# Performance work log

Hardware: AMD Instinct MI355X
Metric: run time of the kernel (lower is better)

Reference implementation:

```python
import jax, jax.numpy as jnp
import numpy as np

NTYPES = 2
B, N, MNEI = 4, 512, 100
M = MNEI * NTYPES          # neighbor slots = maxNeighborNum * ntypes
EMB_LAST = 100             # embedding net sizes [25, 50, 100]
FIT_H = 240
M2 = 16
RMIN, RMAX = 0.5, 6.0


def setup_inputs():
    key = jax.random.key(0)
    ks = jax.random.split(key, 24)
    r = jax.random.uniform(ks[0], (B, N, M), minval=0.6, maxval=7.0)
    v = jax.random.normal(ks[1], (B, N, M, 3))
    v = v / jnp.linalg.norm(v, axis=-1, keepdims=True)
    keep = jax.random.uniform(ks[2], (B, N, M)) < 0.7
    ImageDR = jnp.concatenate([r[..., None], r[..., None] * v], axis=-1)
    ImageDR = jnp.where(keep[..., None], ImageDR, 0.0).astype(jnp.float32)
    Imagetype_map = jax.random.randint(ks[3], (N,), 0, NTYPES)
    list_neigh = jax.random.randint(ks[4], (B, N, M), 0, N + 1)
    type_map = jnp.arange(NTYPES)
    davg = (0.01 * jax.random.normal(ks[5], (NTYPES, M, 4))).astype(jnp.float32)
    dstd = (1.0 + 0.1 * jax.random.uniform(ks[6], (NTYPES, M, 4))).astype(jnp.float32)

    def w(k, shape, fan):
        return (jax.random.normal(k, shape) / np.sqrt(fan)).astype(jnp.float32)

    def b(k, shape):
        return (0.1 * jax.random.normal(k, shape)).astype(jnp.float32)

    emb_W0 = w(ks[7], (NTYPES, NTYPES, 1, 25), 1)
    emb_b0 = b(ks[8], (NTYPES, NTYPES, 25))
    emb_W1 = w(ks[9], (NTYPES, NTYPES, 25, 50), 25)
    emb_b1 = b(ks[10], (NTYPES, NTYPES, 50))
    emb_W2 = w(ks[11], (NTYPES, NTYPES, 50, 100), 50)
    emb_b2 = b(ks[12], (NTYPES, NTYPES, 100))
    fin = M2 * EMB_LAST
    fit_W0 = w(ks[13], (NTYPES, fin, FIT_H), fin)
    fit_b0 = b(ks[14], (NTYPES, FIT_H))
    fit_W1 = w(ks[15], (NTYPES, FIT_H, FIT_H), FIT_H)
    fit_b1 = b(ks[16], (NTYPES, FIT_H))
    fit_W2 = w(ks[17], (NTYPES, FIT_H, FIT_H), FIT_H)
    fit_b2 = b(ks[18], (NTYPES, FIT_H))
    fit_W3 = w(ks[19], (NTYPES, FIT_H, 1), FIT_H)
    fit_b3 = b(ks[20], (NTYPES, 1))
    energy_shift = jnp.array([-3.37, -5.21], dtype=jnp.float32)
    return dict(list_neigh=list_neigh, Imagetype_map=Imagetype_map, type_map=type_map,
                ImageDR=ImageDR, nghost=0, davg=davg, dstd=dstd,
                emb_W0=emb_W0, emb_b0=emb_b0, emb_W1=emb_W1, emb_b1=emb_b1,
                emb_W2=emb_W2, emb_b2=emb_b2,
                fit_W0=fit_W0, fit_b0=fit_b0, fit_W1=fit_W1, fit_b1=fit_b1,
                fit_W2=fit_W2, fit_b2=fit_b2, fit_W3=fit_W3, fit_b3=fit_b3,
                energy_shift=energy_shift)


def _emb(s, W0, b0, W1, b1, W2, b2):
    # DeepPot-SE embedding net with doubling resnet connections
    h = jnp.tanh(s @ W0 + b0)                                   # [..., 25]
    h = jnp.tanh(h @ W1 + b1) + jnp.concatenate([h, h], -1)     # [..., 50]
    return jnp.tanh(h @ W2 + b2) + jnp.concatenate([h, h], -1)  # [..., 100]


def _fit(d, W0, b0, W1, b1, W2, b2, W3, b3):
    h = jnp.tanh(d @ W0 + b0)
    h = h + jnp.tanh(h @ W1 + b1)
    h = h + jnp.tanh(h @ W2 + b2)
    return h @ W3 + b3


def _forward(ImageDR, davg, dstd,
             emb_W0, emb_b0, emb_W1, emb_b1, emb_W2, emb_b2,
             fit_W0, fit_b0, fit_W1, fit_b1, fit_W2, fit_b2, fit_W3, fit_b3,
             energy_shift, Imagetype_map):
    Bsz, Nat, Mtot, _ = ImageDR.shape
    m = Mtot // NTYPES
    R = ImageDR[..., 0]
    Rsafe = jnp.where(R > 1e-5, R, 1.0)
    # smooth switching function s(r): 1/r below Rmin, polynomial taper to Rmax
    u = (R - RMIN) / (RMAX - RMIN)
    mid = (u ** 3 * (-6.0 * u * u + 15.0 * u - 10.0) + 1.0) / Rsafe
    S = jnp.where((R > 0) & (R < RMIN), 1.0 / Rsafe,
                  jnp.where((R > RMIN) & (R < RMAX), mid, 0.0))
    msk = (jnp.abs(R) > 1e-5)[..., None]
    Ri = jnp.concatenate([S[..., None],
                          jnp.where(msk, (S / Rsafe)[..., None] * ImageDR[..., 1:4], 0.0)],
                         axis=-1)                                    # [B,N,M,4] = (s, s*x/r, s*y/r, s*z/r)
    # per-center-type normalization (irregular gather of stats)
    Rn = (Ri - davg[Imagetype_map][None]) / dstd[Imagetype_map][None]
    tmask = [(Imagetype_map == i).astype(Rn.dtype)[None, :, None, None] for i in range(NTYPES)]
    xyz = jnp.zeros((Bsz, Nat, 4, EMB_LAST), Rn.dtype)
    for j in range(NTYPES):                                          # neighbor-type slice
        sl = Rn[:, :, j * m:(j + 1) * m, :]                          # [B,N,m,4]
        s = sl[..., 0:1]
        G = jnp.zeros(sl.shape[:3] + (EMB_LAST,), sl.dtype)
        for i in range(NTYPES):                                      # center type -> pair net (i, j)
            G = G + tmask[i] * _emb(s, emb_W0[i, j], emb_b0[i, j],
                                    emb_W1[i, j], emb_b1[i, j], emb_W2[i, j], emb_b2[i, j])
        xyz = xyz + jnp.einsum('bnmk,bnmc->bnkc', sl, G)
    xyz = xyz / (m * NTYPES)
    # descriptor D = (Ri^T G)^T (Ri^T G)[:, :M2], flattened -> [B,N,EMB_LAST*M2]
    D = jnp.einsum('bnkc,bnkd->bncd', xyz, xyz[..., :M2]).reshape(Bsz, Nat, -1)
    Ei = jnp.zeros((Bsz, Nat), D.dtype)
    for i in range(NTYPES):
        e = _fit(D, fit_W0[i], fit_b0[i], fit_W1[i], fit_b1[i],
                 fit_W2[i], fit_b2[i], fit_W3[i], fit_b3[i])[..., 0] + energy_shift[i]
        Ei = Ei + tmask[i][:, :, 0, 0] * e
    Etot = jnp.sum(Ei, axis=1)
    return Etot, Ei


def reference(list_neigh, Imagetype_map, type_map, ImageDR, nghost, davg, dstd,
              emb_W0, emb_b0, emb_W1, emb_b1, emb_W2, emb_b2,
              fit_W0, fit_b0, fit_W1, fit_b1, fit_W2, fit_b2, fit_W3, fit_b3,
              energy_shift):
    return _forward(ImageDR, davg, dstd,
                    emb_W0, emb_b0, emb_W1, emb_b1, emb_W2, emb_b2,
                    fit_W0, fit_b0, fit_W1, fit_b1, fit_W2, fit_b2, fit_W3, fit_b3,
                    energy_shift, Imagetype_map)
```

## Files before the change

kernel.cpp:

```cpp
#include <hip/hip_runtime.h>
#include <math.h>

#define NT 2
#define BSZ 4
#define NAT 512
#define NATOMS 2048
#define NNEI 200
#define EMB 100
#define FITH 240
#define DDIM 1600
#define TBK 1024

#define BIAS_F  16
#define W3C_F   (BIAS_F + 3 * 512)
#define PERM_I  2064
#define CNT_I   (PERM_I + 2048)
#define USH_BYTE 16512
#define TBL_U   0
#define W0T_U   409600
#define W1T_U   (W0T_U + 819200)
#define W2T_U   (W1T_U + 262144)
#define D_U     (W2T_U + 262144)
#define H0_U    (D_U + 3276800)
#define H1_U    (H0_U + 1048576)
#define USH_END (H1_U + 1048576)
#define WS_NEED ((size_t)USH_BYTE + (size_t)USH_END * 2)

#define N_W0 819200
#define N_W1 262144
#define N_W2 262144
#define N_B  1536
#define N_W3 512
#define N_EI 2048
#define N_WT (N_W0 + N_W1 + N_W2 + N_B + N_W3 + N_EI)
#define WT_BLK ((N_WT + 255) / 256)
#define TB_BLK 512

#define HPAD 264

typedef short s8v __attribute__((ext_vector_type(8)));
typedef float f4v __attribute__((ext_vector_type(4)));

__device__ __forceinline__ float ftanh(float x) {
    float ax = fabsf(x);
    float e = __expf(2.0f * ax);
    float t = 1.0f - __fdividef(2.0f, e + 1.0f);
    return (x < 0.0f) ? -t : t;
}
__device__ __forceinline__ unsigned short f2bf(float f) {
    unsigned u = __float_as_uint(f);
    u += 0x7FFFu + ((u >> 16) & 1u);
    return (unsigned short)(u >> 16);
}
__device__ __forceinline__ float bf2f(unsigned short s) {
    return __uint_as_float(((unsigned)s) << 16);
}
__device__ __forceinline__ float calc_S(float R) {
    float Rsafe = (R > 1e-5f) ? R : 1.0f;
    float u = (R - 0.5f) * (1.0f / 5.5f);
    float uu = u * u;
    float mid = (u * uu * (-6.0f * uu + 15.0f * u - 10.0f) + 1.0f) / Rsafe;
    float S = 0.0f;
    if (R > 0.0f && R < 0.5f)      S = 1.0f / Rsafe;
    else if (R > 0.5f && R < 6.0f) S = mid;
    return S;
}

__global__ void __launch_bounds__(256) prep_kernel(
    const float* __restrict__ fW0, const float* __restrict__ fW1,
    const float* __restrict__ fW2,
    const float* __restrict__ fb0, const float* __restrict__ fb1,
    const float* __restrict__ fb2,
    const float* __restrict__ fW3, const float* __restrict__ fb3,
    const float* __restrict__ eshift,
    const float* __restrict__ davg, const float* __restrict__ dstd,
    const float* __restrict__ eW0, const float* __restrict__ eb0,
    const float* __restrict__ eW1, const float* __restrict__ eb1,
    const float* __restrict__ eW2, const float* __restrict__ eb2,
    const int* __restrict__ itype,
    float* __restrict__ ws, float* __restrict__ out)
{
    __shared__ float los[100], his[100];
    __shared__ float rng[2];
    __shared__ float h0s[8][25];
    __shared__ float h1s[8][50];
    __shared__ int pcnt, poff0, poff1;
    const int tid = threadIdx.x;
    int bxg = blockIdx.x;
    unsigned short* u0 = (unsigned short*)((char*)ws + USH_BYTE);

    if (bxg < WT_BLK) {
        int id = bxg * 256 + tid;
        if (id < N_W0) {
            int n = id / 1600, k = id - n * 1600;
            float v = 0.0f;
            if (n < 240)                  v = fW0[(size_t)k * 240 + n];
            else if (n >= 256 && n < 496) v = fW0[(size_t)(1600 + k) * 240 + (n - 256)];
            u0[W0T_U + id] = f2bf(v);
            return;
        }
        id -= N_W0;
        if (id < N_W1) {
            int n = id / 512, k = id - n * 512;
            float v = 0.0f;
            if (n < 240 && k < 240)       v = fW1[(size_t)k * 240 + n];
            else if (n >= 256 && n < 496 && k >= 256 && k < 496)
                                          v = fW1[(size_t)(240 + (k - 256)) * 240 + (n - 256)];
            u0[W1T_U + id] = f2bf(v);
            return;
        }
        id -= N_W1;
        if (id < N_W2) {
            int n = id / 512, k = id - n * 512;
            float v = 0.0f;
            if (n < 240 && k < 240)       v = fW2[(size_t)k * 240 + n];
            else if (n >= 256 && n < 496 && k >= 256 && k < 496)
                                          v = fW2[(size_t)(240 + (k - 256)) * 240 + (n - 256)];
            u0[W2T_U + id] = f2bf(v);
            return;
        }
        id -= N_W2;
        if (id < N_B) {
            int l = id / 512, n = id - l * 512;
            const float* fb = (l == 0) ? fb0 : (l == 1) ? fb1 : fb2;
            float v = 0.0f;
            if (n < 240)                  v = fb[n];
            else if (n >= 256 && n < 496) v = fb[240 + (n - 256)];
            ws[BIAS_F + l * 512 + n] = v;
            return;
        }
        id -= N_B;
        if (id < N_W3) {
            int n = id;
            float v = 0.0f;
            if (n < 240)                  v = fW3[n];
            else if (n >= 256 && n < 496) v = fW3[240 + (n - 256)];
            ws[W3C_F + n] = v;
            return;
        }
        id -= N_W3;
        if (id < N_EI) {
            int t = itype[id & (NAT - 1)];
            out[4 + id] = fb3[t] + eshift[t];
        }
        return;
    }
    bxg -= WT_BLK;
    if (bxg < TB_BLK) {
        const int nid = bxg >> 7;
        const int kb  = (bxg & 127) * 8;
        const int t = nid >> 1, j = nid & 1;
        if (tid < 100) {
            int m = j * 100 + tid;
            float av = davg[(t * NNEI + m) * 4];
            float sd = dstd[(t * NNEI + m) * 4];
            float inv = __fdividef(1.0f, sd);
            float a = (0.0f - av) * inv;
            float b = (2.0f - av) * inv;
            los[tid] = fminf(a, b);
            his[tid] = fmaxf(a, b);
        }
        __syncthreads();
        if (tid == 0) {
            float lo = los[0], hi = his[0];
            for (int i = 1; i < 100; ++i) { lo = fminf(lo, los[i]); hi = fmaxf(hi, his[i]); }
            rng[0] = lo; rng[1] = hi - lo;
            if (kb == 0) {
                ws[nid * 2] = lo;
                ws[nid * 2 + 1] = (float)(TBK - 1) / (hi - lo);
            }
        }
        __syncthreads();
        const float smin = rng[0], span = rng[1];
        const float* W0 = eW0 + nid * 25;
        const float* B0 = eb0 + nid * 25;
        if (tid < 200) {
            int q = tid / 25, a = tid % 25;
            float s = smin + span * ((float)(kb + q) * (1.0f / (TBK - 1)));
            h0s[q][a] = ftanh(fmaf(s, W0[a], B0[a]));
        }
        __syncthreads();
        const float* W1 = eW1 + nid * 1250;
        const float* B1 = eb1 + nid * 50;
        for (int idx = tid; idx < 400; idx += 256) {
            int q = idx / 50, cc = idx % 50;
            float acc = B1[cc];
#pragma unroll
            for (int a = 0; a < 25; ++a) acc = fmaf(h0s[q][a], W1[a * 50 + cc], acc);
            h1s[q][cc] = ftanh(acc) + h0s[q][(cc < 25) ? cc : cc - 25];
        }
        __syncthreads();
        const float* W2 = eW2 + nid * 5000;
        const float* B2 = eb2 + nid * 100;
        unsigned short* tblu = u0 + TBL_U;
        for (int idx = tid; idx < 800; idx += 256) {
            int q = idx / 100, c = idx % 100;
            float acc = B2[c];
#pragma unroll
            for (int a = 0; a < 50; ++a) acc = fmaf(h1s[q][a], W2[a * 100 + c], acc);
            float g = ftanh(acc) + h1s[q][(c < 50) ? c : c - 50];
            tblu[(size_t)(nid * TBK + kb + q) * 100 + c] = f2bf(g);
        }
        return;
    }
    if (tid == 0) { pcnt = 0; poff0 = 0; poff1 = 0; }
    __syncthreads();
    int* wsi = (int*)ws;
    int local0 = 0;
    for (int i = tid; i < NATOMS; i += 256) local0 += (itype[i & (NAT - 1)] == 0);
    atomicAdd(&pcnt, local0);
    __syncthreads();
    const int c0 = pcnt;
    for (int i = tid; i < NATOMS; i += 256) {
        int t = itype[i & (NAT - 1)];
        int pos = (t == 0) ? atomicAdd(&poff0, 1) : (c0 + atomicAdd(&poff1, 1));
        wsi[PERM_I + pos] = i;
    }
    if (tid == 0) { wsi[CNT_I] = c0; wsi[CNT_I + 1] = NATOMS - c0; }
}

__global__ void __launch_bounds__(128) embed_kernel(
    const int* __restrict__ itype, const float* __restrict__ imagedr,
    const float* __restrict__ davg, const float* __restrict__ dstd,
    float* __restrict__ ws)
{
    __shared__ __align__(16) float4 srn[NNEI];
    __shared__ float sx[NNEI];
    __shared__ float part[2][400];
    const int atom = blockIdx.x;
    const int n = atom & (NAT - 1);
    const int tid = threadIdx.x;
    const int t = itype[n];
    unsigned short* u0 = (unsigned short*)((char*)ws + USH_BYTE);

    const float sm0 = ws[(t * 2 + 0) * 2], sc0 = ws[(t * 2 + 0) * 2 + 1];
    const float sm1 = ws[(t * 2 + 1) * 2], sc1 = ws[(t * 2 + 1) * 2 + 1];

    for (int m = tid; m < NNEI; m += 128) {
        float4 dr = ((const float4*)imagedr)[(size_t)atom * NNEI + m];
        float R = dr.x;
        float S = calc_S(R);
        float Rsafe = (R > 1e-5f) ? R : 1.0f;
        float sr = (fabsf(R) > 1e-5f) ? (S / Rsafe) : 0.0f;
        float4 av = ((const float4*)davg)[t * NNEI + m];
        float4 sd = ((const float4*)dstd)[t * NNEI + m];
        float4 rv;
        rv.x = (S         - av.x) / sd.x;
        rv.y = (sr * dr.y - av.y) / sd.y;
        rv.z = (sr * dr.z - av.z) / sd.z;
        rv.w = (sr * dr.w - av.w) / sd.w;
        srn[m] = rv;
        float smin = (m >= 100) ? sm1 : sm0;
        float scal = (m >= 100) ? sc1 : sc0;
        sx[m] = fminf(fmaxf((rv.x - smin) * scal, 0.0f), (float)(TBK - 2) + 0.9999f);
    }
    __syncthreads();

    const int w = tid >> 6, lane = tid & 63;
    const unsigned short* T = u0 + TBL_U + (size_t)(t * 2 + w) * TBK * EMB;
    const bool hi = (lane < 36);
    float xA0 = 0, xA1 = 0, xA2 = 0, xA3 = 0;
    float xB0 = 0, xB1 = 0, xB2 = 0, xB3 = 0;
#pragma unroll 4
    for (int mi = 0; mi < 100; ++mi) {
        int m = w * 100 + mi;
        float4 rv = srn[m];
        float x = sx[m];
        int i = (int)x;
        float f = x - (float)i;
        const unsigned short* Tr = T + (size_t)i * EMB;
        float g0 = bf2f(Tr[lane]);
        float g1 = bf2f(Tr[EMB + lane]);
        float g = fmaf(f, g1 - g0, g0);
        xA0 = fmaf(rv.x, g, xA0); xA1 = fmaf(rv.y, g, xA1);
        xA2 = fmaf(rv.z, g, xA2); xA3 = fmaf(rv.w, g, xA3);
        if (hi) {
            float h0v = bf2f(Tr[64 + lane]);
            float h1v = bf2f(Tr[EMB + 64 + lane]);
            float g2 = fmaf(f, h1v - h0v, h0v);
            xB0 = fmaf(rv.x, g2, xB0); xB1 = fmaf(rv.y, g2, xB1);
            xB2 = fmaf(rv.z, g2, xB2); xB3 = fmaf(rv.w, g2, xB3);
        }
    }
    part[w][0 * 100 + lane] = xA0; part[w][1 * 100 + lane] = xA1;
    part[w][2 * 100 + lane] = xA2; part[w][3 * 100 + lane] = xA3;
    if (hi) {
        part[w][0 * 100 + 64 + lane] = xB0; part[w][1 * 100 + 64 + lane] = xB1;
        part[w][2 * 100 + 64 + lane] = xB2; part[w][3 * 100 + 64 + lane] = xB3;
    }
    __syncthreads();
    const float inv = 1.0f / 200.0f;
    for (int idx = tid; idx < 400; idx += 128)
        part[0][idx] = (part[0][idx] + part[1][idx]) * inv;
    __syncthreads();
    unsigned short* Drow = u0 + D_U + (size_t)atom * DDIM;
    const float* xt = part[0];
    for (int idx = tid; idx < DDIM; idx += 128) {
        int c = idx >> 4, d = idx & 15;
        float s = xt[c] * xt[d] + xt[100 + c] * xt[100 + d]
                + xt[200 + c] * xt[200 + d] + xt[300 + c] * xt[300 + d];
        Drow[idx] = f2bf(s);
    }
}

__device__ __forceinline__ void fit_gemm256(
    const unsigned short* Hsrc, const unsigned short* Bp,
    int h, int mr, int q, f4v acc[4])
{
#pragma unroll
    for (int kt = 0; kt < 4; ++kt) {
        s8v av = *(const s8v*)((const char*)Hsrc
                 + (size_t)mr * (HPAD * 2) + h * 256 + q * 16 + kt * 64);
#pragma unroll
        for (int j = 0; j < 4; ++j) {
            s8v b = *(const s8v*)(Bp + j * 16 * 512 + kt * 32);
            acc[j] = __builtin_amdgcn_mfma_f32_16x16x32_bf16(av, b, acc[j], 0, 0, 0);
        }
    }
}

__global__ void __launch_bounds__(512) fit_kernel(
    const unsigned short* __restrict__ A,
    const unsigned short* __restrict__ W0T,
    const unsigned short* __restrict__ W1T,
    const unsigned short* __restrict__ W2T,
    const float* __restrict__ biases,
    const float* __restrict__ w3c,
    const int* __restrict__ wsi,
    float* __restrict__ out)
{
    __shared__ float lred[4][64][17];
    __shared__ unsigned short Hs0[16 * HPAD];
    __shared__ unsigned short Hs1[16 * HPAD];
    __shared__ float red2[16][4];

    const int z = blockIdx.y;
    const int cnt = wsi[CNT_I + z];
    const int my = blockIdx.x;
    if (my * 16 >= cnt) return;
    const int base = z ? wsi[CNT_I] : 0;
    const int tid = threadIdx.x;
    const int w = tid >> 6, lane = tid & 63;
    const int mr = lane & 15, q = lane >> 4;
    const int wc = w & 3, h = w >> 2;
    const int n0 = z * 256 + wc * 64;
    const int m0 = my * 16;
    const int arow = wsi[PERM_I + base + min(m0 + mr, cnt - 1)];

    {
        const unsigned short* Ap = A   + (size_t)arow * DDIM + h * 800 + q * 8;
        const unsigned short* Bp = W0T + (size_t)(n0 + mr) * DDIM + h * 800 + q * 8;
        f4v a0 = {0,0,0,0}, a1 = {0,0,0,0}, a2 = {0,0,0,0}, a3 = {0,0,0,0};
#pragma unroll 5
        for (int kt = 0; kt < 25; ++kt) {
            s8v av = *(const s8v*)(Ap + kt * 32);
            s8v b0 = *(const s8v*)(Bp + kt * 32);
            s8v b1 = *(const s8v*)(Bp + 16 * DDIM + kt * 32);
            s8v b2 = *(const s8v*)(Bp + 32 * DDIM + kt * 32);
            s8v b3 = *(const s8v*)(Bp + 48 * DDIM + kt * 32);
            a0 = __builtin_amdgcn_mfma_f32_16x16x32_bf16(av, b0, a0, 0, 0, 0);
            a1 = __builtin_amdgcn_mfma_f32_16x16x32_bf16(av, b1, a1, 0, 0, 0);
            a2 = __builtin_amdgcn_mfma_f32_16x16x32_bf16(av, b2, a2, 0, 0, 0);
            a3 = __builtin_amdgcn_mfma_f32_16x16x32_bf16(av, b3, a3, 0, 0, 0);
        }
        if (h == 1) {
#pragma unroll
            for (int r = 0; r < 4; ++r) {
                lred[wc][lane][r]      = a0[r];
                lred[wc][lane][4 + r]  = a1[r];
                lred[wc][lane][8 + r]  = a2[r];
                lred[wc][lane][12 + r] = a3[r];
            }
        }
        __syncthreads();
        if (h == 0) {
#pragma unroll
            for (int j = 0; j < 4; ++j) {
                const float bv = biases[n0 + j * 16 + mr];
                f4v* ap = (j == 0) ? &a0 : (j == 1) ? &a1 : (j == 2) ? &a2 : &a3;
#pragma unroll
                for (int r = 0; r < 4; ++r) {
                    float s = (*ap)[r] + lred[wc][lane][j * 4 + r] + bv;
                    int row = q * 4 + r, col = wc * 64 + j * 16 + mr;
                    Hs0[row * HPAD + col] = f2bf(ftanh(s));
                }
            }
        }
        __syncthreads();
    }

    {
        const unsigned short* Bp = W1T + (size_t)(n0 + mr) * 512 + z * 256 + h * 128 + q * 8;
        f4v acc[4] = {{0,0,0,0},{0,0,0,0},{0,0,0,0},{0,0,0,0}};
        fit_gemm256(Hs0, Bp, h, mr, q, acc);
        if (h == 1) {
#pragma unroll
            for (int j = 0; j < 4; ++j)
#pragma unroll
                for (int r = 0; r < 4; ++r) lred[wc][lane][j * 4 + r] = acc[j][r];
        }
        __syncthreads();
        if (h == 0) {
#pragma unroll
            for (int j = 0; j < 4; ++j) {
                const float bv = biases[512 + n0 + j * 16 + mr];
#pragma unroll
                for (int r = 0; r < 4; ++r) {
                    float s = acc[j][r] + lred[wc][lane][j * 4 + r] + bv;
                    int row = q * 4 + r, col = wc * 64 + j * 16 + mr;
                    float hv = bf2f(Hs0[row * HPAD + col]) + ftanh(s);
                    Hs1[row * HPAD + col] = f2bf(hv);
                }
            }
        }
        __syncthreads();
    }

    {
        const unsigned short* Bp = W2T + (size_t)(n0 + mr) * 512 + z * 256 + h * 128 + q * 8;
        f4v acc[4] = {{0,0,0,0},{0,0,0,0},{0,0,0,0},{0,0,0,0}};
        fit_gemm256(Hs1, Bp, h, mr, q, acc);
        if (h == 1) {
#pragma unroll
            for (int j = 0; j < 4; ++j)
#pragma unroll
                for (int r = 0; r < 4; ++r) lred[wc][lane][j * 4 + r] = acc[j][r];
        }
        __syncthreads();
        if (h == 0) {
            float pr[4] = {0, 0, 0, 0};
#pragma unroll
            for (int j = 0; j < 4; ++j) {
                const int col = n0 + j * 16 + mr;
                const float bv = biases[1024 + col];
                const float wv = w3c[col];
#pragma unroll
                for (int r = 0; r < 4; ++r) {
                    float s = acc[j][r] + lred[wc][lane][j * 4 + r] + bv;
                    int row = q * 4 + r, coll = wc * 64 + j * 16 + mr;
                    float hv = bf2f(Hs1[row * HPAD + coll]) + ftanh(s);
                    pr[r] = fmaf(hv, wv, pr[r]);
                }
            }
#pragma unroll
            for (int r = 0; r < 4; ++r) {
                float p = pr[r];
                p += __shfl_xor(p, 1, 16);
                p += __shfl_xor(p, 2, 16);
                p += __shfl_xor(p, 4, 16);
                p += __shfl_xor(p, 8, 16);
                if (mr == 0) red2[q * 4 + r][wc] = p;
            }
        }
        __syncthreads();
        if (tid < 16 && m0 + tid < cnt) {
            const int orow = wsi[PERM_I + base + m0 + tid];
            out[4 + orow] += red2[tid][0] + red2[tid][1] + red2[tid][2] + red2[tid][3];
        }
    }
}

__global__ void etot_kernel(float* __restrict__ out) {
    const int b = blockIdx.x;
    float s = 0.0f;
    for (int n = threadIdx.x; n < NAT; n += 256) s += out[4 + b * NAT + n];
#pragma unroll
    for (int off = 32; off > 0; off >>= 1) s += __shfl_down(s, off, 64);
    __shared__ float rr[4];
    if ((threadIdx.x & 63) == 0) rr[threadIdx.x >> 6] = s;
    __syncthreads();
    if (threadIdx.x == 0) out[b] = rr[0] + rr[1] + rr[2] + rr[3];
}

__global__ void dp_atom_kernel(
    const int* __restrict__ itype, const float* __restrict__ imagedr,
    const float* __restrict__ davg, const float* __restrict__ dstd,
    const float* __restrict__ eW0, const float* __restrict__ eb0,
    const float* __restrict__ eW1, const float* __restrict__ eb1,
    const float* __restrict__ eW2, const float* __restrict__ eb2,
    const float* __restrict__ fW0, const float* __restrict__ fb0,
    const float* __restrict__ fW1, const float* __restrict__ fb1,
    const float* __restrict__ fW2, const float* __restrict__ fb2,
    const float* __restrict__ fW3, const float* __restrict__ fb3,
    const float* __restrict__ eshift, float* __restrict__ out)
{
    __shared__ __align__(16) float4 rn4[NNEI];
    __shared__ __align__(16) float  xyz[4 * EMB];
    __shared__ __align__(16) float  h0s[100 * 25];
    __shared__ __align__(16) float  smem[100 * 52];
    const int atom = blockIdx.x;
    const int n = atom & (NAT - 1);
    const int tid = threadIdx.x;
    const int t = itype[n];
    for (int m = tid; m < NNEI; m += 256) {
        float4 dr = ((const float4*)imagedr)[(size_t)atom * NNEI + m];
        float R = dr.x;
        float S = calc_S(R);
        float Rsafe = (R > 1e-5f) ? R : 1.0f;
        float sr = (fabsf(R) > 1e-5f) ? (S / Rsafe) : 0.0f;
        float4 av = ((const float4*)davg)[t * NNEI + m];
        float4 sd = ((const float4*)dstd)[t * NNEI + m];
        float4 rv;
        rv.x = (S - av.x) / sd.x; rv.y = (sr * dr.y - av.y) / sd.y;
        rv.z = (sr * dr.z - av.z) / sd.z; rv.w = (sr * dr.w - av.w) / sd.w;
        rn4[m] = rv;
    }
    const int c = tid & 127; const int mh = tid >> 7;
    float xp0 = 0, xp1 = 0, xp2 = 0, xp3 = 0;
    for (int j = 0; j < NT; ++j) {
        const int wb = t * NT + j;
        const float* W0 = eW0 + wb * 25; const float* B0 = eb0 + wb * 25;
        const float* W1 = eW1 + wb * 1250; const float* B1 = eb1 + wb * 50;
        const float* W2 = eW2 + wb * 5000; const float* B2 = eb2 + wb * 100;
        __syncthreads();
        for (int idx = tid; idx < 2500; idx += 256) {
            int m = idx / 25, a = idx - m * 25;
            h0s[idx] = ftanh(fmaf(rn4[j * 100 + m].x, W0[a], B0[a]));
        }
        __syncthreads();
        for (int idx = tid; idx < 5000; idx += 256) {
            int m = idx / 50, cc = idx - m * 50;
            const float* h0m = h0s + m * 25;
            float acc = B1[cc];
#pragma unroll
            for (int a = 0; a < 25; ++a) acc = fmaf(h0m[a], W1[a * 50 + cc], acc);
            smem[m * 52 + cc] = ftanh(acc) + h0m[(cc < 25) ? cc : cc - 25];
        }
        for (int idx = tid; idx < 200; idx += 256)
            smem[(idx >> 1) * 52 + 50 + (idx & 1)] = 0.0f;
        __syncthreads();
        if (c < EMB) {
            float w2c[52];
#pragma unroll
            for (int a = 0; a < 50; ++a) w2c[a] = W2[a * EMB + c];
            w2c[50] = 0; w2c[51] = 0;
            const float bc = B2[c];
            const int sk = (c < 50) ? c : c - 50;
            for (int i = 0; i < 50; ++i) {
                int m = mh * 50 + i;
                const float* h1m = smem + m * 52;
                float acc = bc;
#pragma unroll
                for (int q = 0; q < 13; ++q) {
                    float4 hv = ((const float4*)h1m)[q];
                    acc = fmaf(hv.x, w2c[4 * q], acc); acc = fmaf(hv.y, w2c[4 * q + 1], acc);
                    acc = fmaf(hv.z, w2c[4 * q + 2], acc); acc = fmaf(hv.w, w2c[4 * q + 3], acc);
                }
                float g = ftanh(acc) + h1m[sk];
                float4 rm = rn4[j * 100 + m];
                xp0 = fmaf(rm.x, g, xp0); xp1 = fmaf(rm.y, g, xp1);
                xp2 = fmaf(rm.z, g, xp2); xp3 = fmaf(rm.w, g, xp3);
            }
        }
    }
    __syncthreads();
    const float inv = 1.0f / 200.0f;
    if (mh == 0 && c < EMB) {
        xyz[c] = xp0 * inv; xyz[EMB + c] = xp1 * inv;
        xyz[2 * EMB + c] = xp2 * inv; xyz[3 * EMB + c] = xp3 * inv;
    }
    __syncthreads();
    if (mh == 1 && c < EMB) {
        xyz[c] += xp0 * inv; xyz[EMB + c] += xp1 * inv;
        xyz[2 * EMB + c] += xp2 * inv; xyz[3 * EMB + c] += xp3 * inv;
    }
    __syncthreads();
    float* Dld = smem;
    for (int idx = tid; idx < DDIM; idx += 256) {
        int cc = idx >> 4, d = idx & 15;
        Dld[idx] = xyz[cc] * xyz[d] + xyz[EMB + cc] * xyz[EMB + d]
                 + xyz[2 * EMB + cc] * xyz[2 * EMB + d] + xyz[3 * EMB + cc] * xyz[3 * EMB + d];
    }
    __syncthreads();
    float* hA = smem + DDIM; float* hB = hA + FITH; float* h2 = hB + FITH; float* red = h2 + FITH;
    if (tid < FITH) {
        const float* W = fW0 + (size_t)t * DDIM * FITH;
        float acc = fb0[t * FITH + tid];
        for (int f = 0; f < DDIM; f += 4) {
            float4 dv = *(const float4*)(Dld + f);
            acc = fmaf(dv.x, W[f * FITH + tid], acc); acc = fmaf(dv.y, W[(f + 1) * FITH + tid], acc);
            acc = fmaf(dv.z, W[(f + 2) * FITH + tid], acc); acc = fmaf(dv.w, W[(f + 3) * FITH + tid], acc);
        }
        hA[tid] = ftanh(acc);
    }
    __syncthreads();
    if (tid < FITH) {
        const float* W = fW1 + t * FITH * FITH;
        float acc = fb1[t * FITH + tid];
        for (int f = 0; f < FITH; f += 4) {
            float4 hv = *(const float4*)(hA + f);
            acc = fmaf(hv.x, W[f * FITH + tid], acc); acc = fmaf(hv.y, W[(f + 1) * FITH + tid], acc);
            acc = fmaf(hv.z, W[(f + 2) * FITH + tid], acc); acc = fmaf(hv.w, W[(f + 3) * FITH + tid], acc);
        }
        hB[tid] = hA[tid] + ftanh(acc);
    }
    __syncthreads();
    if (tid < FITH) {
        const float* W = fW2 + t * FITH * FITH;
        float acc = fb2[t * FITH + tid];
        for (int f = 0; f < FITH; f += 4) {
            float4 hv = *(const float4*)(hB + f);
            acc = fmaf(hv.x, W[f * FITH + tid], acc); acc = fmaf(hv.y, W[(f + 1) * FITH + tid], acc);
            acc = fmaf(hv.z, W[(f + 2) * FITH + tid], acc); acc = fmaf(hv.w, W[(f + 3) * FITH + tid], acc);
        }
        h2[tid] = hB[tid] + ftanh(acc);
    }
    __syncthreads();
    float p = (tid < FITH) ? h2[tid] * fW3[t * FITH + tid] : 0.0f;
#pragma unroll
    for (int off = 32; off > 0; off >>= 1) p += __shfl_down(p, off, 64);
    if ((tid & 63) == 0) red[tid >> 6] = p;
    __syncthreads();
    if (tid == 0) out[4 + atom] = red[0] + red[1] + red[2] + red[3] + fb3[t] + eshift[t];
}

extern "C" void kernel_launch(void* const* d_in, const int* in_sizes, int n_in,
                              void* d_out, int out_size, void* d_ws, size_t ws_size,
                              hipStream_t stream) {
    const int*   itype   = (const int*)  d_in[1];
    const float* imagedr = (const float*)d_in[3];
    const float* davg    = (const float*)d_in[5];
    const float* dstd    = (const float*)d_in[6];
    const float* eW0     = (const float*)d_in[7];
    const float* eb0     = (const float*)d_in[8];
    const float* eW1     = (const float*)d_in[9];
    const float* eb1     = (const float*)d_in[10];
    const float* eW2     = (const float*)d_in[11];
    const float* eb2     = (const float*)d_in[12];
    const float* fW0     = (const float*)d_in[13];
    const float* fb0     = (const float*)d_in[14];
    const float* fW1     = (const float*)d_in[15];
    const float* fb1     = (const float*)d_in[16];
    const float* fW2     = (const float*)d_in[17];
    const float* fb2     = (const float*)d_in[18];
    const float* fW3     = (const float*)d_in[19];
    const float* fb3     = (const float*)d_in[20];
    const float* eshift  = (const float*)d_in[21];
    float* out = (float*)d_out;
    float* ws  = (float*)d_ws;

    if (ws_size >= WS_NEED) {
        unsigned short* u0 = (unsigned short*)((char*)ws + USH_BYTE);
        const int* wsi = (const int*)ws;
        prep_kernel<<<WT_BLK + TB_BLK + 1, 256, 0, stream>>>(
            fW0, fW1, fW2, fb0, fb1, fb2, fW3, fb3, eshift,
            davg, dstd, eW0, eb0, eW1, eb1, eW2, eb2, itype, ws, out);
        embed_kernel<<<NATOMS, 128, 0, stream>>>(itype, imagedr, davg, dstd, ws);
        fit_kernel<<<dim3(128, 2), 512, 0, stream>>>(
            u0 + D_U, u0 + W0T_U, u0 + W1T_U, u0 + W2T_U,
            ws + BIAS_F, ws + W3C_F, wsi, out);
        etot_kernel<<<BSZ, 256, 0, stream>>>(out);
    } else {
        dp_atom_kernel<<<NATOMS, 256, 0, stream>>>(itype, imagedr, davg, dstd,
            eW0, eb0, eW1, eb1, eW2, eb2,
            fW0, fb0, fW1, fb1, fW2, fb2, fW3, fb3, eshift, out);
        etot_kernel<<<BSZ, 256, 0, stream>>>(out);
    }
}
```

Before: 193.7 us.

## Pre-swizzle fit weights and descriptors into MFMA fragment order with type-sorted rows

Weight transposes now write the fit weights directly in the per-lane MFMA fragment layout (16-column blocks by 32-k tiles by 64 lanes by 8 elements). The embed kernel uses an inverse permutation to write each atom's descriptor into a type-sorted, 16-row-padded fragment layout. The fit kernel can then load A and B operands as fully contiguous 1 KB chunks per wave instead of strided rows, and no longer needs an indirect row gather. This adds an inverse-permutation array and a padded descriptor buffer, and relies on correct padding between the two type groups.

New measurement: 179.9 us. -7.2%, faster.

```diff
diff --git a/kernel.cpp b/kernel.cpp
--- a/kernel.cpp
+++ b/kernel.cpp
@@ -14,16 +14,16 @@
 #define BIAS_F  16
 #define W3C_F   (BIAS_F + 3 * 512)
 #define PERM_I  2064
-#define CNT_I   (PERM_I + 2048)
-#define USH_BYTE 16512
+#define CNT_I   (PERM_I + 2064)
+#define IPERM_I (CNT_I + 4)
+#define USH_BYTE 24832
 #define TBL_U   0
 #define W0T_U   409600
 #define W1T_U   (W0T_U + 819200)
 #define W2T_U   (W1T_U + 262144)
 #define D_U     (W2T_U + 262144)
-#define H0_U    (D_U + 3276800)
-#define H1_U    (H0_U + 1048576)
-#define USH_END (H1_U + 1048576)
+#define D_SZ    (129 * 50 * 512)
+#define USH_END (D_U + D_SZ)
 #define WS_NEED ((size_t)USH_BYTE + (size_t)USH_END * 2)
 
 #define N_W0 819200
@@ -92,7 +92,11 @@
     if (bxg < WT_BLK) {
         int id = bxg * 256 + tid;
         if (id < N_W0) {
-            int n = id / 1600, k = id - n * 1600;
+            int e = id & 7, lane = (id >> 3) & 63;
+            int rem = id >> 9;
+            int kt = rem % 50, c16 = rem / 50;
+            int n = c16 * 16 + (lane & 15);
+            int k = kt * 32 + (lane >> 4) * 8 + e;
             float v = 0.0f;
             if (n < 240)                  v = fW0[(size_t)k * 240 + n];
             else if (n >= 256 && n < 496) v = fW0[(size_t)(1600 + k) * 240 + (n - 256)];
@@ -101,7 +105,11 @@
         }
         id -= N_W0;
         if (id < N_W1) {
-            int n = id / 512, k = id - n * 512;
+            int e = id & 7, lane = (id >> 3) & 63;
+            int rem = id >> 9;
+            int kt = rem & 15, c16 = rem >> 4;
+            int n = c16 * 16 + (lane & 15);
+            int k = kt * 32 + (lane >> 4) * 8 + e;
             float v = 0.0f;
             if (n < 240 && k < 240)       v = fW1[(size_t)k * 240 + n];
             else if (n >= 256 && n < 496 && k >= 256 && k < 496)
@@ -111,7 +119,11 @@
         }
         id -= N_W1;
         if (id < N_W2) {
-            int n = id / 512, k = id - n * 512;
+            int e = id & 7, lane = (id >> 3) & 63;
+            int rem = id >> 9;
+            int kt = rem & 15, c16 = rem >> 4;
+            int n = c16 * 16 + (lane & 15);
+            int k = kt * 32 + (lane >> 4) * 8 + e;
             float v = 0.0f;
             if (n < 240 && k < 240)       v = fW2[(size_t)k * 240 + n];
             else if (n >= 256 && n < 496 && k >= 256 && k < 496)
@@ -211,12 +223,16 @@
     atomicAdd(&pcnt, local0);
     __syncthreads();
     const int c0 = pcnt;
+    const int c0p = (c0 + 15) & ~15;
     for (int i = tid; i < NATOMS; i += 256) {
         int t = itype[i & (NAT - 1)];
-        int pos = (t == 0) ? atomicAdd(&poff0, 1) : (c0 + atomicAdd(&poff1, 1));
+        int pos = (t == 0) ? atomicAdd(&poff0, 1) : (c0p + atomicAdd(&poff1, 1));
         wsi[PERM_I + pos] = i;
-    }
-    if (tid == 0) { wsi[CNT_I] = c0; wsi[CNT_I + 1] = NATOMS - c0; }
+        wsi[IPERM_I + i] = pos;
+    }
+    if (tid == 0) {
+        wsi[CNT_I] = c0; wsi[CNT_I + 1] = NATOMS - c0; wsi[CNT_I + 2] = c0p;
+    }
 }
 
 __global__ void __launch_bounds__(128) embed_kernel(
@@ -232,6 +248,7 @@
     const int tid = threadIdx.x;
     const int t = itype[n];
     unsigned short* u0 = (unsigned short*)((char*)ws + USH_BYTE);
+    const int* wsi = (const int*)ws;
 
     const float sm0 = ws[(t * 2 + 0) * 2], sc0 = ws[(t * 2 + 0) * 2 + 1];
     const float sm1 = ws[(t * 2 + 1) * 2], sc1 = ws[(t * 2 + 1) * 2 + 1];
@@ -293,37 +310,31 @@
     for (int idx = tid; idx < 400; idx += 128)
         part[0][idx] = (part[0][idx] + part[1][idx]) * inv;
     __syncthreads();
-    unsigned short* Drow = u0 + D_U + (size_t)atom * DDIM;
+    const int p = wsi[IPERM_I + atom];
+    const int rb = p >> 4, mrp = p & 15;
+    unsigned short* Df = u0 + D_U;
     const float* xt = part[0];
-    for (int idx = tid; idx < DDIM; idx += 128) {
-        int c = idx >> 4, d = idx & 15;
-        float s = xt[c] * xt[d] + xt[100 + c] * xt[100 + d]
-                + xt[200 + c] * xt[200 + d] + xt[300 + c] * xt[300 + d];
-        Drow[idx] = f2bf(s);
-    }
-}
-
-__device__ __forceinline__ void fit_gemm256(
-    const unsigned short* Hsrc, const unsigned short* Bp,
-    int h, int mr, int q, f4v acc[4])
-{
-#pragma unroll
-    for (int kt = 0; kt < 4; ++kt) {
-        s8v av = *(const s8v*)((const char*)Hsrc
-                 + (size_t)mr * (HPAD * 2) + h * 256 + q * 16 + kt * 64);
-#pragma unroll
-        for (int j = 0; j < 4; ++j) {
-            s8v b = *(const s8v*)(Bp + j * 16 * 512 + kt * 32);
-            acc[j] = __builtin_amdgcn_mfma_f32_16x16x32_bf16(av, b, acc[j], 0, 0, 0);
-        }
+    for (int k8 = tid; k8 < 200; k8 += 128) {
+        int k = k8 * 8;
+        int c = k >> 4, d0 = k & 15;
+        int kt = k >> 5, q = (k >> 3) & 3;
+        s8v pack;
+#pragma unroll
+        for (int e = 0; e < 8; ++e) {
+            int d = d0 + e;
+            float s = xt[c] * xt[d] + xt[100 + c] * xt[100 + d]
+                    + xt[200 + c] * xt[200 + d] + xt[300 + c] * xt[300 + d];
+            ((unsigned short*)&pack)[e] = f2bf(s);
+        }
+        *(s8v*)(Df + ((size_t)(rb * 50 + kt) * 64 + q * 16 + mrp) * 8) = pack;
     }
 }
 
 __global__ void __launch_bounds__(512) fit_kernel(
-    const unsigned short* __restrict__ A,
-    const unsigned short* __restrict__ W0T,
-    const unsigned short* __restrict__ W1T,
-    const unsigned short* __restrict__ W2T,
+    const unsigned short* __restrict__ Af,
+    const unsigned short* __restrict__ W0F,
+    const unsigned short* __restrict__ W1F,
+    const unsigned short* __restrict__ W2F,
     const float* __restrict__ biases,
     const float* __restrict__ w3c,
     const int* __restrict__ wsi,
@@ -338,76 +349,91 @@
     const int cnt = wsi[CNT_I + z];
     const int my = blockIdx.x;
     if (my * 16 >= cnt) return;
-    const int base = z ? wsi[CNT_I] : 0;
+    const int basep = z ? wsi[CNT_I + 2] : 0;
     const int tid = threadIdx.x;
     const int w = tid >> 6, lane = tid & 63;
     const int mr = lane & 15, q = lane >> 4;
     const int wc = w & 3, h = w >> 2;
     const int n0 = z * 256 + wc * 64;
     const int m0 = my * 16;
-    const int arow = wsi[PERM_I + base + min(m0 + mr, cnt - 1)];
-
+    const int rb = (basep >> 4) + my;
+    const int c16b = z * 16 + wc * 4;
+
+    f4v a0 = {0,0,0,0}, a1 = {0,0,0,0}, a2 = {0,0,0,0}, a3 = {0,0,0,0};
     {
-        const unsigned short* Ap = A   + (size_t)arow * DDIM + h * 800 + q * 8;
-        const unsigned short* Bp = W0T + (size_t)(n0 + mr) * DDIM + h * 800 + q * 8;
-        f4v a0 = {0,0,0,0}, a1 = {0,0,0,0}, a2 = {0,0,0,0}, a3 = {0,0,0,0};
+        const unsigned short* Ap = Af  + ((size_t)(rb * 50 + h * 25) * 64 + lane) * 8;
+        const unsigned short* Bp = W0F + ((size_t)(c16b * 50 + h * 25) * 64 + lane) * 8;
 #pragma unroll 5
         for (int kt = 0; kt < 25; ++kt) {
-            s8v av = *(const s8v*)(Ap + kt * 32);
-            s8v b0 = *(const s8v*)(Bp + kt * 32);
-            s8v b1 = *(const s8v*)(Bp + 16 * DDIM + kt * 32);
-            s8v b2 = *(const s8v*)(Bp + 32 * DDIM + kt * 32);
-            s8v b3 = *(const s8v*)(Bp + 48 * DDIM + kt * 32);
+            s8v av = *(const s8v*)(Ap + kt * 512);
+            s8v b0 = *(const s8v*)(Bp + kt * 512);
+            s8v b1 = *(const s8v*)(Bp + 25600 + kt * 512);
+            s8v b2 = *(const s8v*)(Bp + 51200 + kt * 512);
+            s8v b3 = *(const s8v*)(Bp + 76800 + kt * 512);
             a0 = __builtin_amdgcn_mfma_f32_16x16x32_bf16(av, b0, a0, 0, 0, 0);
             a1 = __builtin_amdgcn_mfma_f32_16x16x32_bf16(av, b1, a1, 0, 0, 0);
             a2 = __builtin_amdgcn_mfma_f32_16x16x32_bf16(av, b2, a2, 0, 0, 0);
             a3 = __builtin_amdgcn_mfma_f32_16x16x32_bf16(av, b3, a3, 0, 0, 0);
         }
+    }
+    if (h == 1) {
+#pragma unroll
+        for (int r = 0; r < 4; ++r) {
+            lred[wc][lane][r]      = a0[r];
+            lred[wc][lane][4 + r]  = a1[r];
+            lred[wc][lane][8 + r]  = a2[r];
+            lred[wc][lane][12 + r] = a3[r];
+        }
+    }
+    __syncthreads();
+    if (h == 0) {
+#pragma unroll
+        for (int j = 0; j < 4; ++j) {
+            const float bv = biases[n0 + j * 16 + mr];
+            f4v* ap = (j == 0) ? &a0 : (j == 1) ? &a1 : (j == 2) ? &a2 : &a3;
+            const int col = wc * 64 + j * 16 + mr;
+#pragma unroll
+            for (int r = 0; r < 4; ++r) {
+                float s = (*ap)[r] + lred[wc][lane][j * 4 + r] + bv;
+                int row = q * 4 + r;
+                Hs0[row * HPAD + col] = f2bf(ftanh(s));
+            }
+        }
+    }
+    __syncthreads();
+
+    {
+        const unsigned short* Bp = W1F + ((size_t)(c16b * 16 + z * 8 + h * 4) * 64 + lane) * 8;
+        f4v ac[4] = {{0,0,0,0},{0,0,0,0},{0,0,0,0},{0,0,0,0}};
+#pragma unroll
+        for (int kt = 0; kt < 4; ++kt) {
+            s8v av = *(const s8v*)((const char*)Hs0
+                     + (size_t)mr * (HPAD * 2) + h * 256 + q * 16 + kt * 64);
+            s8v b0 = *(const s8v*)(Bp + kt * 512);
+            s8v b1 = *(const s8v*)(Bp + 8192 + kt * 512);
+            s8v b2 = *(const s8v*)(Bp + 16384 + kt * 512);
+            s8v b3 = *(const s8v*)(Bp + 24576 + kt * 512);
+            ac[0] = __builtin_amdgcn_mfma_f32_16x16x32_bf16(av, b0, ac[0], 0, 0, 0);
+            ac[1] = __builtin_amdgcn_mfma_f32_16x16x32_bf16(av, b1, ac[1], 0, 0, 0);
+            ac[2] = __builtin_amdgcn_mfma_f32_16x16x32_bf16(av, b2, ac[2], 0, 0, 0);
+            ac[3] = __builtin_amdgcn_mfma_f32_16x16x32_bf16(av, b3, ac[3], 0, 0, 0);
+        }
         if (h == 1) {
 #pragma unroll
-            for (int r = 0; r < 4; ++r) {
-                lred[wc][lane][r]      = a0[r];
-                lred[wc][lane][4 + r]  = a1[r];
-                lred[wc][lane][8 + r]  = a2[r];
-                lred[wc][lane][12 + r] = a3[r];
-            }
-        }
-        __syncthreads();
-        if (h == 0) {
-#pragma unroll
-            for (int j = 0; j < 4; ++j) {
-                const float bv = biases[n0 + j * 16 + mr];
-                f4v* ap = (j == 0) ? &a0 : (j == 1) ? &a1 : (j == 2) ? &a2 : &a3;
-#pragma unroll
-                for (int r = 0; r < 4; ++r) {
-                    float s = (*ap)[r] + lred[wc][lane][j * 4 + r] + bv;
-                    int row = q * 4 + r, col = wc * 64 + j * 16 + mr;
-                    Hs0[row * HPAD + col] = f2bf(ftanh(s));
-                }
-            }
-        }
-        __syncthreads();
-    }
-
-    {
-        const unsigned short* Bp = W1T + (size_t)(n0 + mr) * 512 + z * 256 + h * 128 + q * 8;
-        f4v acc[4] = {{0,0,0,0},{0,0,0,0},{0,0,0,0},{0,0,0,0}};
-        fit_gemm256(Hs0, Bp, h, mr, q, acc);
-        if (h == 1) {
-#pragma unroll
             for (int j = 0; j < 4; ++j)
 #pragma unroll
-                for (int r = 0; r < 4; ++r) lred[wc][lane][j * 4 + r] = acc[j][r];
+                for (int r = 0; r < 4; ++r) lred[wc][lane][j * 4 + r] = ac[j][r];
         }
         __syncthreads();
         if (h == 0) {
 #pragma unroll
             for (int j = 0; j < 4; ++j) {
                 const float bv = biases[512 + n0 + j * 16 + mr];
+                const int col = wc * 64 + j * 16 + mr;
 #pragma unroll
                 for (int r = 0; r < 4; ++r) {
-                    float s = acc[j][r] + lred[wc][lane][j * 4 + r] + bv;
-                    int row = q * 4 + r, col = wc * 64 + j * 16 + mr;
+                    float s = ac[j][r] + lred[wc][lane][j * 4 + r] + bv;
+                    int row = q * 4 + r;
                     float hv = bf2f(Hs0[row * HPAD + col]) + ftanh(s);
                     Hs1[row * HPAD + col] = f2bf(hv);
                 }
@@ -417,14 +443,26 @@
     }
 
     {
-        const unsigned short* Bp = W2T + (size_t)(n0 + mr) * 512 + z * 256 + h * 128 + q * 8;
-        f4v acc[4] = {{0,0,0,0},{0,0,0,0},{0,0,0,0},{0,0,0,0}};
-        fit_gemm256(Hs1, Bp, h, mr, q, acc);
+        const unsigned short* Bp = W2F + ((size_t)(c16b * 16 + z * 8 + h * 4) * 64 + lane) * 8;
+        f4v ac[4] = {{0,0,0,0},{0,0,0,0},{0,0,0,0},{0,0,0,0}};
+#pragma unroll
+        for (int kt = 0; kt < 4; ++kt) {
+            s8v av = *(const s8v*)((const char*)Hs1
+                     + (size_t)mr * (HPAD * 2) + h * 256 + q * 16 + kt * 64);
+            s8v b0 = *(const s8v*)(Bp + kt * 512);
+            s8v b1 = *(const s8v*)(Bp + 8192 + kt * 512);
+            s8v b2 = *(const s8v*)(Bp + 16384 + kt * 512);
+            s8v b3 = *(const s8v*)(Bp + 24576 + kt * 512);
+            ac[0] = __builtin_amdgcn_mfma_f32_16x16x32_bf16(av, b0, ac[0], 0, 0, 0);
+            ac[1] = __builtin_amdgcn_mfma_f32_16x16x32_bf16(av, b1, ac[1], 0, 0, 0);
+            ac[2] = __builtin_amdgcn_mfma_f32_16x16x32_bf16(av, b2, ac[2], 0, 0, 0);
+            ac[3] = __builtin_amdgcn_mfma_f32_16x16x32_bf16(av, b3, ac[3], 0, 0, 0);
+        }
         if (h == 1) {
 #pragma unroll
             for (int j = 0; j < 4; ++j)
 #pragma unroll
-                for (int r = 0; r < 4; ++r) lred[wc][lane][j * 4 + r] = acc[j][r];
+                for (int r = 0; r < 4; ++r) lred[wc][lane][j * 4 + r] = ac[j][r];
         }
         __syncthreads();
         if (h == 0) {
@@ -434,10 +472,11 @@
                 const int col = n0 + j * 16 + mr;
                 const float bv = biases[1024 + col];
                 const float wv = w3c[col];
+                const int coll = wc * 64 + j * 16 + mr;
 #pragma unroll
                 for (int r = 0; r < 4; ++r) {
-                    float s = acc[j][r] + lred[wc][lane][j * 4 + r] + bv;
-                    int row = q * 4 + r, coll = wc * 64 + j * 16 + mr;
+                    float s = ac[j][r] + lred[wc][lane][j * 4 + r] + bv;
+                    int row = q * 4 + r;
                     float hv = bf2f(Hs1[row * HPAD + coll]) + ftanh(s);
                     pr[r] = fmaf(hv, wv, pr[r]);
                 }
@@ -454,7 +493,7 @@
         }
         __syncthreads();
         if (tid < 16 && m0 + tid < cnt) {
-            const int orow = wsi[PERM_I + base + m0 + tid];
+            const int orow = wsi[PERM_I + basep + m0 + tid];
             out[4 + orow] += red2[tid][0] + red2[tid][1] + red2[tid][2] + red2[tid][3];
         }
     }
```
